# Optimization experiments

Hardware: AMD Instinct MI355X
Metric: run time of the kernel (lower is better)

The kernel has to match this reference:

```python
import jax, jax.numpy as jnp
import numpy as np

D_MODEL = 1024
NUM_HEADS = 16
D_K = D_MODEL // NUM_HEADS
SCALE = 1.0 / np.sqrt(D_K).astype(np.float32)
MASK_FILL = -10000.0


def setup_inputs() -> dict:
    key = jax.random.key(0)
    ks = jax.random.split(key, 5)
    B, S = 2, 2048
    x = jax.random.normal(ks[0], (B, S, D_MODEL), dtype=jnp.float32)
    mask = jax.random.randint(ks[1], (B, S), 0, 2, dtype=jnp.int32)
    # Kaiming-uniform-ish init like nn.Linear defaults
    lim1 = 1.0 / np.sqrt(D_MODEL)
    Wqkv = jax.random.uniform(ks[2], (D_MODEL, 3 * D_MODEL), jnp.float32, -lim1, lim1)
    bqkv = jnp.zeros((3 * D_MODEL,), jnp.float32)
    Wout = jax.random.uniform(ks[3], (D_MODEL, D_MODEL), jnp.float32, -lim1, lim1)
    bout = jnp.zeros((D_MODEL,), jnp.float32)
    return {"x": x, "mask": mask, "Wqkv": Wqkv, "bqkv": bqkv, "Wout": Wout, "bout": bout}


def reference(x, mask, Wqkv, bqkv, Wout, bout):
    B, S, _ = x.shape
    qkv = (x @ Wqkv + bqkv).reshape(B, S, 3, NUM_HEADS, D_K)
    qkv = jnp.transpose(qkv, (2, 0, 3, 1, 4))
    q, k, v = qkv[0], qkv[1], qkv[2]
    # scaled dot-product scores [B,H,S,S]
    scores = jnp.einsum("bhqd,bhkd->bhqk", q, k) * SCALE
    # key-padding mask [B,S] -> [B,1,1,S]; masked positions set to -10000 (as in source)
    m = mask[:, None, None, :]
    scores = jnp.where(m == 0, MASK_FILL, scores)
    attn = jax.nn.softmax(scores, axis=-1)
    # dropout is disabled (eval/inference)
    context = jnp.einsum("bhqk,bhkd->bhqd", attn, v)
    context = jnp.transpose(context, (0, 2, 1, 3)).reshape(B, S, D_MODEL)
    return context @ Wout + bout
```

## Files before the change

### kernel.cpp

```cpp
#include <hip/hip_runtime.h>

typedef _Float16 f16;
typedef _Float16 f16x2 __attribute__((ext_vector_type(2)));
typedef _Float16 f16x4 __attribute__((ext_vector_type(4)));
typedef _Float16 f16x8 __attribute__((ext_vector_type(8)));
typedef float    f32x4 __attribute__((ext_vector_type(4)));
typedef float    f32x16 __attribute__((ext_vector_type(16)));
typedef int      i32x4 __attribute__((ext_vector_type(4)));

#define NHEADS 16
#define DK 64
#define BATCH 2
#define SEQ 2048
#define DMODEL 1024
#define MTOT (BATCH*SEQ)
#define NQKV (3*DMODEL)
#define NBH  (BATCH*NHEADS)
#define LOG2E 1.44269504f
#define QSCALE (0.125f * LOG2E)
#define MASKVAL (-10000.0f * LOG2E)

__device__ inline f16x8 ld_f16x8_g(const f16* p) {
  return __builtin_bit_cast(f16x8, *reinterpret_cast<const i32x4*>(p));
}

__device__ inline f16x2 cvt_pk(float a, float b) {
  return __builtin_bit_cast(f16x2, __builtin_amdgcn_cvt_pkrtz(a, b));
}

__device__ inline void gl_lds16(const void* g, void* l) {
  __builtin_amdgcn_global_load_lds(
      (const __attribute__((address_space(1))) unsigned int*)g,
      (__attribute__((address_space(3))) unsigned int*)l, 16, 0, 0);
}

__device__ inline int sigma_k(int s) {
  return (s & ~12) | ((s & 4) << 1) | ((s & 8) >> 1);
}

__device__ inline void tcvt_tile(float (*tile)[33], const float* __restrict__ in,
                                 f16* __restrict__ out, int K, int N, int k0, int n0) {
  const int t = threadIdx.x, tx = t & 31, ty = t >> 5;
  #pragma unroll
  for (int i = 0; i < 4; ++i)
    tile[ty + 8*i][tx] = in[(size_t)(k0 + ty + 8*i) * N + n0 + tx];
  __syncthreads();
  #pragma unroll
  for (int i = 0; i < 4; ++i)
    out[(size_t)(n0 + ty + 8*i) * K + k0 + tx] = (f16)tile[tx][ty + 8*i];
}

__global__ __launch_bounds__(256) void k_prep(
    const float* __restrict__ x, f16* __restrict__ xh,
    const float* __restrict__ Wqkv, f16* __restrict__ Wqkvt,
    const float* __restrict__ Wout, f16* __restrict__ Woutt,
    const int* __restrict__ mask, int* __restrict__ inv, int* __restrict__ cnt)
{
  __shared__ float tile[32][33];
  __shared__ int part[256];
  const int bid = blockIdx.x;
  const int t = threadIdx.x;
  if (bid < 4096) {
    int i = (bid * 256 + t) * 4;
    float4 v = *reinterpret_cast<const float4*>(x + i);
    f16x4 o = { (f16)v.x, (f16)v.y, (f16)v.z, (f16)v.w };
    *reinterpret_cast<f16x4*>(xh + i) = o;
  } else if (bid < 4096 + 3072) {
    int tl = bid - 4096;
    tcvt_tile(tile, Wqkv, Wqkvt, DMODEL, NQKV, (tl / 96) * 32, (tl % 96) * 32);
  } else if (bid < 8192) {
    int tl = bid - 4096 - 3072;
    tcvt_tile(tile, Wout, Woutt, DMODEL, DMODEL, (tl / 32) * 32, (tl % 32) * 32);
  } else {
    const int b = bid - 8192;
    const int* mp = mask + b * SEQ;
    int* iv = inv + b * SEQ;
    const int base = t * 8;
    int m[8]; int s = 0;
    #pragma unroll
    for (int i = 0; i < 8; ++i) { m[i] = mp[base + i]; s += (m[i] != 0); }
    part[t] = s;
    __syncthreads();
    for (int d = 1; d < 256; d <<= 1) {
      int v = (t >= d) ? part[t - d] : 0;
      __syncthreads();
      part[t] += v;
      __syncthreads();
    }
    int pos = (t == 0) ? 0 : part[t - 1];
    #pragma unroll
    for (int i = 0; i < 8; ++i) {
      if (m[i] != 0) { iv[pos] = base + i; ++pos; }
    }
    if (t == 255) cnt[b] = part[255];
  }
}

__global__ __launch_bounds__(256, 2) void k_gemm_qkv2(
    const f16* __restrict__ A, const f16* __restrict__ Bt,
    const float* __restrict__ bias, const int* __restrict__ inv,
    const int* __restrict__ cnt,
    f16* __restrict__ qo, f16* __restrict__ ko, f16* __restrict__ vto, int K)
{
  __shared__ f16 As[64][64];
  __shared__ f16 Bs[128][64];
  const int bid = blockIdx.x;
  const bool isQ = bid < 512;

  const int t = threadIdx.x;
  const int l = t & 63, w = t >> 6;
  const int lc = l & 15, g = l >> 4;
  const int srow = l >> 3;
  const int ssl  = ((l & 7) ^ srow) * 16;
  const int swz  = (lc & 7) << 4;

  int m0, n0, b = 0, c = 0;
  const f16* Btp;
  const float* biasp;
  size_t aoff[2];
  if (isQ) {
    n0 = (bid & 7) * 128;  m0 = (bid >> 3) * 64;
    Btp = Bt;  biasp = bias;
    #pragma unroll
    for (int it = 0; it < 2; ++it)
      aoff[it] = (size_t)(m0 + it*32 + w*8 + srow) * K;
  } else {
    const int idx = bid - 512;
    n0 = (idx & 15) * 128;  m0 = (idx >> 4) * 64;
    b = m0 >> 11;
    const int sl0 = m0 & (SEQ - 1);
    c = cnt[b];
    if (sl0 >= ((c + 63) & ~63)) return;
    Btp = Bt + (size_t)DMODEL * DMODEL;
    biasp = bias + DMODEL;
    #pragma unroll
    for (int it = 0; it < 2; ++it) {
      int slot = sl0 + it*32 + w*8 + srow;
      int sidx = (slot < c) ? slot : (c > 0 ? c - 1 : 0);
      aoff[it] = (size_t)(b * SEQ + (inv[b * SEQ + sidx] & (SEQ - 1))) * K;
    }
  }

  f32x4 acc[4][2] = {};

  for (int kt = 0; kt < K; kt += 64) {
    __syncthreads();
    #pragma unroll
    for (int it = 0; it < 2; ++it)
      gl_lds16((const char*)(A + aoff[it] + kt) + ssl, &As[it*32 + w*8][0]);
    #pragma unroll
    for (int it = 0; it < 4; ++it) {
      int row = it*32 + w*8 + srow;
      gl_lds16((const char*)(Btp + (size_t)(n0 + row) * K + kt) + ssl,
               &Bs[it*32 + w*8][0]);
    }
    __syncthreads();

    #pragma unroll
    for (int ks = 0; ks < 64; ks += 32) {
      f16x8 af[4], bf[2];
      #pragma unroll
      for (int i = 0; i < 4; ++i)
        af[i] = *(const f16x8*)((const char*)&As[i*16 + lc][0] + ((ks*2 + g*16) ^ swz));
      #pragma unroll
      for (int j = 0; j < 2; ++j)
        bf[j] = *(const f16x8*)((const char*)&Bs[w*32 + j*16 + lc][0] + ((ks*2 + g*16) ^ swz));
      #pragma unroll
      for (int i = 0; i < 4; ++i)
        #pragma unroll
        for (int j = 0; j < 2; ++j)
          acc[i][j] = __builtin_amdgcn_mfma_f32_16x16x32_f16(af[i], bf[j], acc[i][j], 0, 0, 0);
    }
  }

  if (isQ) {
    #pragma unroll
    for (int i = 0; i < 4; ++i) {
      const int row0 = m0 + i*16 + g*4;
      const int qb = row0 >> 11, s0 = row0 & (SEQ - 1);
      #pragma unroll
      for (int j = 0; j < 2; ++j) {
        int col = n0 + w*32 + j*16 + lc;
        float bv = biasp[col];
        int h = col >> 6, d = col & 63;
        size_t bh = (size_t)(qb * NHEADS + h);
        #pragma unroll
        for (int r = 0; r < 4; ++r)
          qo[(bh * SEQ + s0 + r) * DK + d] = (f16)((acc[i][j][r] + bv) * QSCALE);
      }
    }
  } else {
    const int sl0 = m0 & (SEQ - 1);
    #pragma unroll
    for (int i = 0; i < 4; ++i) {
      const int slot0 = sl0 + i*16 + g*4;
      #pragma unroll
      for (int j = 0; j < 2; ++j) {
        int colkv = n0 + w*32 + j*16 + lc;
        float bv = biasp[colkv];
        int kv = colkv >> 10;
        int h = (colkv >> 6) & 15, d = colkv & 63;
        size_t bh = (size_t)(b * NHEADS + h);
        if (kv == 0) {
          #pragma unroll
          for (int r = 0; r < 4; ++r)
            ko[(bh * SEQ + slot0 + r) * DK + d] = (f16)(acc[i][j][r] + bv);
        } else {
          union { f16x2 h2[2]; f16x4 h4; } u;
          u.h2[0] = cvt_pk(acc[i][j][0] + bv, acc[i][j][1] + bv);
          u.h2[1] = cvt_pk(acc[i][j][2] + bv, acc[i][j][3] + bv);
          *(f16x4*)(vto + (bh * DK + d) * SEQ + sigma_k(slot0)) = u.h4;
        }
      }
    }
  }
}

__global__ __launch_bounds__(256, 2) void k_gemm_out(
    const f16* __restrict__ A, const f16* __restrict__ Bt,
    const float* __restrict__ bias, float* __restrict__ outf, int N, int K)
{
  __shared__ f16 As[64][64];
  __shared__ f16 Bs[128][64];
  const int m0 = blockIdx.y * 64, n0 = blockIdx.x * 128;
  const int t = threadIdx.x;
  const int l = t & 63, w = t >> 6;
  const int lc = l & 15, g = l >> 4;
  const int srow = l >> 3;
  const int ssl  = ((l & 7) ^ srow) * 16;
  const int swz  = (lc & 7) << 4;

  f32x4 acc[4][2] = {};

  for (int kt = 0; kt < K; kt += 64) {
    __syncthreads();
    #pragma unroll
    for (int it = 0; it < 2; ++it) {
      int row = it*32 + w*8 + srow;
      gl_lds16((const char*)(A + (size_t)(m0 + row) * K + kt) + ssl,
               &As[it*32 + w*8][0]);
    }
    #pragma unroll
    for (int it = 0; it < 4; ++it) {
      int row = it*32 + w*8 + srow;
      gl_lds16((const char*)(Bt + (size_t)(n0 + row) * K + kt) + ssl,
               &Bs[it*32 + w*8][0]);
    }
    __syncthreads();

    #pragma unroll
    for (int ks = 0; ks < 64; ks += 32) {
      f16x8 af[4], bf[2];
      #pragma unroll
      for (int i = 0; i < 4; ++i)
        af[i] = *(const f16x8*)((const char*)&As[i*16 + lc][0] + ((ks*2 + g*16) ^ swz));
      #pragma unroll
      for (int j = 0; j < 2; ++j)
        bf[j] = *(const f16x8*)((const char*)&Bs[w*32 + j*16 + lc][0] + ((ks*2 + g*16) ^ swz));
      #pragma unroll
      for (int i = 0; i < 4; ++i)
        #pragma unroll
        for (int j = 0; j < 2; ++j)
          acc[i][j] = __builtin_amdgcn_mfma_f32_16x16x32_f16(af[i], bf[j], acc[i][j], 0, 0, 0);
    }
  }

  #pragma unroll
  for (int i = 0; i < 4; ++i) {
    #pragma unroll
    for (int j = 0; j < 2; ++j) {
      int col = n0 + w*32 + j*16 + lc;
      float bv = bias[col];
      #pragma unroll
      for (int r = 0; r < 4; ++r) {
        int row = m0 + i*16 + g*4 + r;
        outf[(size_t)row * N + col] = acc[i][j][r] + bv;
      }
    }
  }
}

__global__ __launch_bounds__(256, 2) void k_attn10(
    const f16* __restrict__ Q, const f16* __restrict__ K,
    const f16* __restrict__ Vt, const int* __restrict__ cnt,
    f16* __restrict__ ctx)
{
  __shared__ f16 Kb[2][32][128];
  __shared__ f16 Vb[2][32][128];

  const int bid = blockIdx.x;
  const int xcd = bid & 7, slot = bid >> 3;
  const int bh = xcd * 4 + (slot >> 4);
  const int qb = slot & 15;
  const int b  = bh >> 4, h = bh & (NHEADS - 1);
  const int t = threadIdx.x, l = t & 63, w = t >> 6;
  const int r31 = l & 31, hi = l >> 5;
  const int Rm = r31 & 15;
  const int q0 = qb * 128 + w * 32;

  const int c = cnt[b];
  const int NTc = (c + 63) >> 6;

  const f16* Qp = Q + (size_t)bh * SEQ * DK;
  const f16* Kp = K + (size_t)bh * SEQ * DK;
  const f16* Vp = Vt + (size_t)bh * DK * SEQ;

  f16x8 qf[4];
  #pragma unroll
  for (int ds = 0; ds < 4; ++ds)
    qf[ds] = ld_f16x8_g(Qp + (size_t)(q0 + r31) * DK + ds*16 + hi*8);

  f32x16 o[2] = {};
  float mrow = -3e38f;
  float lsum = 0.f;

  auto stage = [&](int buf, int kt) {
    #pragma unroll
    for (int cc = 0; cc < 2; ++cc) {
      int Rbase = w*8 + cc*4;
      int R = Rbase + (l >> 4);
      int u = (l & 15) ^ (R & 15);
      int off32 = (u >> 3) * 32;
      int byteoff = (u & 7) * 16;
      gl_lds16((const char*)Kp + (size_t)(kt + off32 + R) * (DK*2) + byteoff,
               &Kb[buf][Rbase][0]);
      gl_lds16((const char*)Vp + (size_t)(off32 + R) * (SEQ*2) + (size_t)kt*2 + byteoff,
               &Vb[buf][Rbase][0]);
    }
  };

  stage(0, 0);

  for (int it = 0; it < NTc; ++it) {
    __syncthreads();
    if (it + 1 < NTc) stage((it + 1) & 1, (it + 1) * 64);
    const int kt = it * 64;
    const char* kb = (const char*)&Kb[it & 1][0][0];
    const char* vb = (const char*)&Vb[it & 1][0][0];

    f32x16 p[2];
    if (kt + 64 <= c) {
      #pragma unroll
      for (int T = 0; T < 2; ++T)
        #pragma unroll
        for (int r = 0; r < 16; ++r) p[T][r] = 0.f;
    } else {
      #pragma unroll
      for (int T = 0; T < 2; ++T)
        #pragma unroll
        for (int r = 0; r < 16; ++r) {
          int k = kt + T*32 + 4*hi + (r & 3) + 8*(r >> 2);
          p[T][r] = (k < c) ? 0.f : MASKVAL;
        }
    }

    __builtin_amdgcn_s_setprio(1);
    #pragma unroll
    for (int T = 0; T < 2; ++T)
      #pragma unroll
      for (int ds = 0; ds < 4; ++ds) {
        int slotc = T*8 + ds*2 + hi;
        f16x8 kf = *(const f16x8*)(kb + r31*256 + ((slotc ^ Rm) << 4));
        p[T] = __builtin_amdgcn_mfma_f32_32x32x16_f16(kf, qf[ds], p[T], 0, 0, 0);
      }
    __builtin_amdgcn_s_setprio(0);

    float mx;
    {
      f32x4 t4;
      #pragma unroll
      for (int r = 0; r < 4; ++r)
        t4[r] = fmaxf(fmaxf(p[0][r], p[0][r+4]), fmaxf(p[0][r+8], p[0][r+12]));
      #pragma unroll
      for (int r = 0; r < 4; ++r)
        t4[r] = fmaxf(t4[r], fmaxf(fmaxf(p[1][r], p[1][r+4]), fmaxf(p[1][r+8], p[1][r+12])));
      mx = fmaxf(fmaxf(t4[0], t4[1]), fmaxf(t4[2], t4[3]));
    }
    mx = fmaxf(mx, __shfl_xor(mx, 32));

    if (!__all(mx <= mrow + 8.f)) {
      float nm = fmaxf(mrow, mx);
      float sc = __builtin_amdgcn_exp2f(mrow - nm);
      mrow = nm;
      lsum *= sc;
      #pragma unroll
      for (int dt = 0; dt < 2; ++dt)
        #pragma unroll
        for (int r = 0; r < 16; ++r) o[dt][r] *= sc;
    }

    f16x2 h2[2][8];
    float s0 = 0.f, s1 = 0.f;
    #pragma unroll
    for (int T = 0; T < 2; ++T)
      #pragma unroll
      for (int rp = 0; rp < 8; ++rp) {
        float e0 = __builtin_amdgcn_exp2f(p[T][2*rp]   - mrow);
        float e1 = __builtin_amdgcn_exp2f(p[T][2*rp+1] - mrow);
        s0 += e0; s1 += e1;
        h2[T][rp] = cvt_pk(e0, e1);
      }
    lsum += s0 + s1;

    __builtin_amdgcn_s_setprio(1);
    #pragma unroll
    for (int T = 0; T < 2; ++T)
      #pragma unroll
      for (int half = 0; half < 2; ++half) {
        union { f16x2 a[4]; f16x8 v8; } pu;
        pu.a[0] = h2[T][half*4+0]; pu.a[1] = h2[T][half*4+1];
        pu.a[2] = h2[T][half*4+2]; pu.a[3] = h2[T][half*4+3];
        int m = T*2 + half;
        #pragma unroll
        for (int dt = 0; dt < 2; ++dt) {
          int slotc = dt*8 + m*2 + hi;
          f16x8 vf = *(const f16x8*)(vb + r31*256 + ((slotc ^ Rm) << 4));
          o[dt] = __builtin_amdgcn_mfma_f32_32x32x16_f16(vf, pu.v8, o[dt], 0, 0, 0);
        }
      }
    __builtin_amdgcn_s_setprio(0);
  }

  lsum += __shfl_xor(lsum, 32);
  float inv = 1.f / lsum;
  f16* cp = ctx + (size_t)(b*SEQ + q0 + r31) * DMODEL + h*DK;
  #pragma unroll
  for (int dt = 0; dt < 2; ++dt)
    #pragma unroll
    for (int rq = 0; rq < 4; ++rq) {
      union { f16x2 h2v[2]; f16x4 h4v; } u;
      u.h2v[0] = cvt_pk(o[dt][4*rq+0]*inv, o[dt][4*rq+1]*inv);
      u.h2v[1] = cvt_pk(o[dt][4*rq+2]*inv, o[dt][4*rq+3]*inv);
      *(f16x4*)(cp + dt*32 + 8*rq + 4*hi) = u.h4v;
    }
}

extern "C" void kernel_launch(void* const* d_in, const int* in_sizes, int n_in,
                              void* d_out, int out_size, void* d_ws, size_t ws_size,
                              hipStream_t stream) {
  const float* x    = (const float*)d_in[0];
  const int*   mask = (const int*)d_in[1];
  const float* Wqkv = (const float*)d_in[2];
  const float* bqkv = (const float*)d_in[3];
  const float* Wout = (const float*)d_in[4];
  const float* bout = (const float*)d_in[5];
  float* out = (float*)d_out;

  const size_t SZ_X    = (size_t)MTOT * DMODEL * 2;
  const size_t SZ_WQKV = (size_t)NQKV * DMODEL * 2;
  const size_t SZ_WOUT = (size_t)DMODEL * DMODEL * 2;
  const size_t SZ_QKV  = (size_t)BATCH * NHEADS * SEQ * DK * 2;
  const size_t SZ_INV  = (size_t)MTOT * 4;
  const size_t SZ_CNT  = 256;
  const size_t NEED = SZ_X + SZ_WQKV + SZ_WOUT + 3*SZ_QKV + SZ_X + SZ_INV + SZ_CNT;
  if (ws_size < NEED) return;

  char* p = (char*)d_ws;
  f16* xh    = (f16*)p; p += SZ_X;
  f16* Wqkvt = (f16*)p; p += SZ_WQKV;
  f16* Woutt = (f16*)p; p += SZ_WOUT;
  f16* Qh    = (f16*)p; p += SZ_QKV;
  f16* Kh    = (f16*)p; p += SZ_QKV;
  f16* Vth   = (f16*)p; p += SZ_QKV;
  f16* ctx   = (f16*)p; p += SZ_X;
  int* inv   = (int*)p; p += SZ_INV;
  int* cnt   = (int*)p; p += SZ_CNT;

  k_prep<<<4096 + 3072 + 1024 + BATCH, 256, 0, stream>>>(
      x, xh, Wqkv, Wqkvt, Wout, Woutt, mask, inv, cnt);

  k_gemm_qkv2<<<512 + 1024, 256, 0, stream>>>(
      xh, Wqkvt, bqkv, inv, cnt, Qh, Kh, Vth, DMODEL);

  k_attn10<<<32 * 16, 256, 0, stream>>>(Qh, Kh, Vth, cnt, ctx);

  k_gemm_out<<<dim3(DMODEL/128, MTOT/64), 256, 0, stream>>>(
      ctx, Woutt, bout, out, DMODEL, DMODEL);
}
```

Measured before the change: 97.73 us.

## Double-buffer GEMM LDS tiles, widen attention staging, vectorize weight transpose

Both GEMM kernels get double-buffered LDS with a prefetch of the next K tile issued before computing the current one, which cuts one barrier per iteration and overlaps global loads with MFMA work. The attention kernel now stages two 64-key tiles per period, halving barrier count, and the weight transpose-convert uses float4 loads and packed f16x4 stores. In exchange, LDS per block doubles in every kernel (48KB for the GEMMs, 64KB for attention), which may limit occupancy.

```diff
diff --git a/kernel.cpp b/kernel.cpp
--- a/kernel.cpp
+++ b/kernel.cpp
@@ -40,14 +40,15 @@
 
 __device__ inline void tcvt_tile(float (*tile)[33], const float* __restrict__ in,
                                  f16* __restrict__ out, int K, int N, int k0, int n0) {
-  const int t = threadIdx.x, tx = t & 31, ty = t >> 5;
-  #pragma unroll
-  for (int i = 0; i < 4; ++i)
-    tile[ty + 8*i][tx] = in[(size_t)(k0 + ty + 8*i) * N + n0 + tx];
+  const int t = threadIdx.x, j = t & 7, ty = t >> 3;
+  float4 v = *reinterpret_cast<const float4*>(in + (size_t)(k0 + ty) * N + n0 + j*4);
+  tile[ty][j*4+0] = v.x; tile[ty][j*4+1] = v.y;
+  tile[ty][j*4+2] = v.z; tile[ty][j*4+3] = v.w;
   __syncthreads();
-  #pragma unroll
-  for (int i = 0; i < 4; ++i)
-    out[(size_t)(n0 + ty + 8*i) * K + k0 + tx] = (f16)tile[tx][ty + 8*i];
+  union { f16x2 h2[2]; f16x4 h4; } u;
+  u.h2[0] = cvt_pk(tile[j*4+0][ty], tile[j*4+1][ty]);
+  u.h2[1] = cvt_pk(tile[j*4+2][ty], tile[j*4+3][ty]);
+  *(f16x4*)(out + (size_t)(n0 + ty) * K + k0 + j*4) = u.h4;
 }
 
 __global__ __launch_bounds__(256) void k_prep(
@@ -102,8 +103,8 @@
     const int* __restrict__ cnt,
     f16* __restrict__ qo, f16* __restrict__ ko, f16* __restrict__ vto, int K)
 {
-  __shared__ f16 As[64][64];
-  __shared__ f16 Bs[128][64];
+  __shared__ f16 As[2][64][64];
+  __shared__ f16 Bs[2][128][64];
   const int bid = blockIdx.x;
   const bool isQ = bid < 512;
 
@@ -141,30 +142,36 @@
     }
   }
 
-  f32x4 acc[4][2] = {};
-
-  for (int kt = 0; kt < K; kt += 64) {
-    __syncthreads();
+  auto stage = [&](int buf, int kt) {
     #pragma unroll
     for (int it = 0; it < 2; ++it)
-      gl_lds16((const char*)(A + aoff[it] + kt) + ssl, &As[it*32 + w*8][0]);
+      gl_lds16((const char*)(A + aoff[it] + kt) + ssl, &As[buf][it*32 + w*8][0]);
     #pragma unroll
     for (int it = 0; it < 4; ++it) {
       int row = it*32 + w*8 + srow;
       gl_lds16((const char*)(Btp + (size_t)(n0 + row) * K + kt) + ssl,
-               &Bs[it*32 + w*8][0]);
-    }
+               &Bs[buf][it*32 + w*8][0]);
+    }
+  };
+
+  f32x4 acc[4][2] = {};
+  const int NTk = K >> 6;
+  stage(0, 0);
+
+  for (int ti = 0; ti < NTk; ++ti) {
     __syncthreads();
-
+    if (ti + 1 < NTk) stage((ti + 1) & 1, (ti + 1) * 64);
+    const char* abase = (const char*)&As[ti & 1][0][0];
+    const char* bbase = (const char*)&Bs[ti & 1][0][0];
     #pragma unroll
     for (int ks = 0; ks < 64; ks += 32) {
       f16x8 af[4], bf[2];
       #pragma unroll
       for (int i = 0; i < 4; ++i)
-        af[i] = *(const f16x8*)((const char*)&As[i*16 + lc][0] + ((ks*2 + g*16) ^ swz));
+        af[i] = *(const f16x8*)(abase + (i*16 + lc)*128 + ((ks*2 + g*16) ^ swz));
       #pragma unroll
       for (int j = 0; j < 2; ++j)
-        bf[j] = *(const f16x8*)((const char*)&Bs[w*32 + j*16 + lc][0] + ((ks*2 + g*16) ^ swz));
+        bf[j] = *(const f16x8*)(bbase + (w*32 + j*16 + lc)*128 + ((ks*2 + g*16) ^ swz));
       #pragma unroll
       for (int i = 0; i < 4; ++i)
         #pragma unroll
@@ -220,8 +227,8 @@
     const f16* __restrict__ A, const f16* __restrict__ Bt,
     const float* __restrict__ bias, float* __restrict__ outf, int N, int K)
 {
-  __shared__ f16 As[64][64];
-  __shared__ f16 Bs[128][64];
+  __shared__ f16 As[2][64][64];
+  __shared__ f16 Bs[2][128][64];
   const int m0 = blockIdx.y * 64, n0 = blockIdx.x * 128;
   const int t = threadIdx.x;
   const int l = t & 63, w = t >> 6;
@@ -230,33 +237,39 @@
   const int ssl  = ((l & 7) ^ srow) * 16;
   const int swz  = (lc & 7) << 4;
 
-  f32x4 acc[4][2] = {};
-
-  for (int kt = 0; kt < K; kt += 64) {
-    __syncthreads();
+  auto stage = [&](int buf, int kt) {
     #pragma unroll
     for (int it = 0; it < 2; ++it) {
       int row = it*32 + w*8 + srow;
       gl_lds16((const char*)(A + (size_t)(m0 + row) * K + kt) + ssl,
-               &As[it*32 + w*8][0]);
+               &As[buf][it*32 + w*8][0]);
     }
     #pragma unroll
     for (int it = 0; it < 4; ++it) {
       int row = it*32 + w*8 + srow;
       gl_lds16((const char*)(Bt + (size_t)(n0 + row) * K + kt) + ssl,
-               &Bs[it*32 + w*8][0]);
-    }
+               &Bs[buf][it*32 + w*8][0]);
+    }
+  };
+
+  f32x4 acc[4][2] = {};
+  const int NTk = K >> 6;
+  stage(0, 0);
+
+  for (int ti = 0; ti < NTk; ++ti) {
     __syncthreads();
-
+    if (ti + 1 < NTk) stage((ti + 1) & 1, (ti + 1) * 64);
+    const char* abase = (const char*)&As[ti & 1][0][0];
+    const char* bbase = (const char*)&Bs[ti & 1][0][0];
     #pragma unroll
     for (int ks = 0; ks < 64; ks += 32) {
       f16x8 af[4], bf[2];
       #pragma unroll
       for (int i = 0; i < 4; ++i)
-        af[i] = *(const f16x8*)((const char*)&As[i*16 + lc][0] + ((ks*2 + g*16) ^ swz));
+        af[i] = *(const f16x8*)(abase + (i*16 + lc)*128 + ((ks*2 + g*16) ^ swz));
       #pragma unroll
       for (int j = 0; j < 2; ++j)
-        bf[j] = *(const f16x8*)((const char*)&Bs[w*32 + j*16 + lc][0] + ((ks*2 + g*16) ^ swz));
+        bf[j] = *(const f16x8*)(bbase + (w*32 + j*16 + lc)*128 + ((ks*2 + g*16) ^ swz));
       #pragma unroll
       for (int i = 0; i < 4; ++i)
         #pragma unroll
@@ -280,13 +293,13 @@
   }
 }
 
-__global__ __launch_bounds__(256, 2) void k_attn10(
+__global__ __launch_bounds__(256, 2) void k_attn11(
     const f16* __restrict__ Q, const f16* __restrict__ K,
     const f16* __restrict__ Vt, const int* __restrict__ cnt,
     f16* __restrict__ ctx)
 {
-  __shared__ f16 Kb[2][32][128];
-  __shared__ f16 Vb[2][32][128];
+  __shared__ f16 Kb[2][2][32][128];
+  __shared__ f16 Vb[2][2][32][128];
 
   const int bid = blockIdx.x;
   const int xcd = bid & 7, slot = bid >> 3;
@@ -300,6 +313,7 @@
 
   const int c = cnt[b];
   const int NTc = (c + 63) >> 6;
+  const int NP  = (NTc + 1) >> 1;
 
   const f16* Qp = Q + (size_t)bh * SEQ * DK;
   const f16* Kp = K + (size_t)bh * SEQ * DK;
@@ -314,111 +328,124 @@
   float mrow = -3e38f;
   float lsum = 0.f;
 
-  auto stage = [&](int buf, int kt) {
-    #pragma unroll
-    for (int cc = 0; cc < 2; ++cc) {
-      int Rbase = w*8 + cc*4;
-      int R = Rbase + (l >> 4);
-      int u = (l & 15) ^ (R & 15);
-      int off32 = (u >> 3) * 32;
-      int byteoff = (u & 7) * 16;
-      gl_lds16((const char*)Kp + (size_t)(kt + off32 + R) * (DK*2) + byteoff,
-               &Kb[buf][Rbase][0]);
-      gl_lds16((const char*)Vp + (size_t)(off32 + R) * (SEQ*2) + (size_t)kt*2 + byteoff,
-               &Vb[buf][Rbase][0]);
+  auto stage_period = [&](int buf, int pp) {
+    #pragma unroll
+    for (int j2 = 0; j2 < 2; ++j2) {
+      int tile = pp*2 + j2;
+      if (tile >= NTc) break;
+      int kt = tile * 64;
+      #pragma unroll
+      for (int cc = 0; cc < 2; ++cc) {
+        int Rbase = w*8 + cc*4;
+        int R = Rbase + (l >> 4);
+        int u = (l & 15) ^ (R & 15);
+        int off32 = (u >> 3) * 32;
+        int byteoff = (u & 7) * 16;
+        gl_lds16((const char*)Kp + (size_t)(kt + off32 + R) * (DK*2) + byteoff,
+                 &Kb[buf][j2][Rbase][0]);
+        gl_lds16((const char*)Vp + (size_t)(off32 + R) * (SEQ*2) + (size_t)kt*2 + byteoff,
+                 &Vb[buf][j2][Rbase][0]);
+      }
     }
   };
 
-  stage(0, 0);
-
-  for (int it = 0; it < NTc; ++it) {
+  stage_period(0, 0);
+
+  for (int pp = 0; pp < NP; ++pp) {
     __syncthreads();
-    if (it + 1 < NTc) stage((it + 1) & 1, (it + 1) * 64);
-    const int kt = it * 64;
-    const char* kb = (const char*)&Kb[it & 1][0][0];
-    const char* vb = (const char*)&Vb[it & 1][0][0];
-
-    f32x16 p[2];
-    if (kt + 64 <= c) {
+    if (pp + 1 < NP) stage_period((pp + 1) & 1, pp + 1);
+    const int buf = pp & 1;
+
+    #pragma unroll
+    for (int j2 = 0; j2 < 2; ++j2) {
+      const int tile = pp*2 + j2;
+      if (tile >= NTc) break;
+      const int kt = tile * 64;
+      const char* kb = (const char*)&Kb[buf][j2][0][0];
+      const char* vb = (const char*)&Vb[buf][j2][0][0];
+
+      f32x16 p[2];
+      if (kt + 64 <= c) {
+        #pragma unroll
+        for (int T = 0; T < 2; ++T)
+          #pragma unroll
+          for (int r = 0; r < 16; ++r) p[T][r] = 0.f;
+      } else {
+        #pragma unroll
+        for (int T = 0; T < 2; ++T)
+          #pragma unroll
+          for (int r = 0; r < 16; ++r) {
+            int k = kt + T*32 + 4*hi + (r & 3) + 8*(r >> 2);
+            p[T][r] = (k < c) ? 0.f : MASKVAL;
+          }
+      }
+
+      __builtin_amdgcn_s_setprio(1);
       #pragma unroll
       for (int T = 0; T < 2; ++T)
         #pragma unroll
-        for (int r = 0; r < 16; ++r) p[T][r] = 0.f;
-    } else {
+        for (int ds = 0; ds < 4; ++ds) {
+          int slotc = T*8 + ds*2 + hi;
+          f16x8 kf = *(const f16x8*)(kb + r31*256 + ((slotc ^ Rm) << 4));
+          p[T] = __builtin_amdgcn_mfma_f32_32x32x16_f16(kf, qf[ds], p[T], 0, 0, 0);
+        }
+      __builtin_amdgcn_s_setprio(0);
+
+      float mx;
+      {
+        f32x4 t4;
+        #pragma unroll
+        for (int r = 0; r < 4; ++r)
+          t4[r] = fmaxf(fmaxf(p[0][r], p[0][r+4]), fmaxf(p[0][r+8], p[0][r+12]));
+        #pragma unroll
+        for (int r = 0; r < 4; ++r)
+          t4[r] = fmaxf(t4[r], fmaxf(fmaxf(p[1][r], p[1][r+4]), fmaxf(p[1][r+8], p[1][r+12])));
+        mx = fmaxf(fmaxf(t4[0], t4[1]), fmaxf(t4[2], t4[3]));
+      }
+      mx = fmaxf(mx, __shfl_xor(mx, 32));
+
+      if (!__all(mx <= mrow + 8.f)) {
+        float nm = fmaxf(mrow, mx);
+        float sc = __builtin_amdgcn_exp2f(mrow - nm);
+        mrow = nm;
+        lsum *= sc;
+        #pragma unroll
+        for (int dt = 0; dt < 2; ++dt)
+          #pragma unroll
+          for (int r = 0; r < 16; ++r) o[dt][r] *= sc;
+      }
+
+      f16x2 h2[2][8];
+      float s0 = 0.f, s1 = 0.f;
       #pragma unroll
       for (int T = 0; T < 2; ++T)
         #pragma unroll
-        for (int r = 0; r < 16; ++r) {
-          int k = kt + T*32 + 4*hi + (r & 3) + 8*(r >> 2);
-          p[T][r] = (k < c) ? 0.f : MASKVAL;
+        for (int rp = 0; rp < 8; ++rp) {
+          float e0 = __builtin_amdgcn_exp2f(p[T][2*rp]   - mrow);
+          float e1 = __builtin_amdgcn_exp2f(p[T][2*rp+1] - mrow);
+          s0 += e0; s1 += e1;
+          h2[T][rp] = cvt_pk(e0, e1);
         }
-    }
-
-    __builtin_amdgcn_s_setprio(1);
-    #pragma unroll
-    for (int T = 0; T < 2; ++T)
-      #pragma unroll
-      for (int ds = 0; ds < 4; ++ds) {
-        int slotc = T*8 + ds*2 + hi;
-        f16x8 kf = *(const f16x8*)(kb + r31*256 + ((slotc ^ Rm) << 4));
-        p[T] = __builtin_amdgcn_mfma_f32_32x32x16_f16(kf, qf[ds], p[T], 0, 0, 0);
-      }
-    __builtin_amdgcn_s_setprio(0);
-
-    float mx;
-    {
-      f32x4 t4;
-      #pragma unroll
-      for (int r = 0; r < 4; ++r)
-        t4[r] = fmaxf(fmaxf(p[0][r], p[0][r+4]), fmaxf(p[0][r+8], p[0][r+12]));
-      #pragma unroll
-      for (int r = 0; r < 4; ++r)
-        t4[r] = fmaxf(t4[r], fmaxf(fmaxf(p[1][r], p[1][r+4]), fmaxf(p[1][r+8], p[1][r+12])));
-      mx = fmaxf(fmaxf(t4[0], t4[1]), fmaxf(t4[2], t4[3]));
-    }
-    mx = fmaxf(mx, __shfl_xor(mx, 32));
-
-    if (!__all(mx <= mrow + 8.f)) {
-      float nm = fmaxf(mrow, mx);
-      float sc = __builtin_amdgcn_exp2f(mrow - nm);
-      mrow = nm;
-      lsum *= sc;
-      #pragma unroll
-      for (int dt = 0; dt < 2; ++dt)
-        #pragma unroll
-        for (int r = 0; r < 16; ++r) o[dt][r] *= sc;
-    }
-
-    f16x2 h2[2][8];
-    float s0 = 0.f, s1 = 0.f;
-    #pragma unroll
-    for (int T = 0; T < 2; ++T)
-      #pragma unroll
-      for (int rp = 0; rp < 8; ++rp) {
-        float e0 = __builtin_amdgcn_exp2f(p[T][2*rp]   - mrow);
-        float e1 = __builtin_amdgcn_exp2f(p[T][2*rp+1] - mrow);
-        s0 += e0; s1 += e1;
-        h2[T][rp] = cvt_pk(e0, e1);
-      }
-    lsum += s0 + s1;
-
-    __builtin_amdgcn_s_setprio(1);
-    #pragma unroll
-    for (int T = 0; T < 2; ++T)
-      #pragma unroll
-      for (int half = 0; half < 2; ++half) {
-        union { f16x2 a[4]; f16x8 v8; } pu;
-        pu.a[0] = h2[T][half*4+0]; pu.a[1] = h2[T][half*4+1];
-        pu.a[2] = h2[T][half*4+2]; pu.a[3] = h2[T][half*4+3];
-        int m = T*2 + half;
-        #pragma unroll
-        for (int dt = 0; dt < 2; ++dt) {
-          int slotc = dt*8 + m*2 + hi;
-          f16x8 vf = *(const f16x8*)(vb + r31*256 + ((slotc ^ Rm) << 4));
-          o[dt] = __builtin_amdgcn_mfma_f32_32x32x16_f16(vf, pu.v8, o[dt], 0, 0, 0);
+      lsum += s0 + s1;
+
+      __builtin_amdgcn_s_setprio(1);
+      #pragma unroll
+      for (int T = 0; T < 2; ++T)
+        #pragma unroll
+        for (int half = 0; half < 2; ++half) {
+          union { f16x2 a[4]; f16x8 v8; } pu;
+          pu.a[0] = h2[T][half*4+0]; pu.a[1] = h2[T][half*4+1];
+          pu.a[2] = h2[T][half*4+2]; pu.a[3] = h2[T][half*4+3];
+          int m = T*2 + half;
+          #pragma unroll
+          for (int dt = 0; dt < 2; ++dt) {
+            int slotc = dt*8 + m*2 + hi;
+            f16x8 vf = *(const f16x8*)(vb + r31*256 + ((slotc ^ Rm) << 4));
+            o[dt] = __builtin_amdgcn_mfma_f32_32x32x16_f16(vf, pu.v8, o[dt], 0, 0, 0);
+          }
         }
-      }
-    __builtin_amdgcn_s_setprio(0);
+      __builtin_amdgcn_s_setprio(0);
+    }
   }
 
   lsum += __shfl_xor(lsum, 32);
@@ -472,7 +499,7 @@
   k_gemm_qkv2<<<512 + 1024, 256, 0, stream>>>(
       xh, Wqkvt, bqkv, inv, cnt, Qh, Kh, Vth, DMODEL);
 
-  k_attn10<<<32 * 16, 256, 0, stream>>>(Qh, Kh, Vth, cnt, ctx);
+  k_attn11<<<32 * 16, 256, 0, stream>>>(Qh, Kh, Vth, cnt, ctx);
 
   k_gemm_out<<<dim3(DMODEL/128, MTOT/64), 256, 0, stream>>>(
       ctx, Woutt, bout, out, DMODEL, DMODEL);
```

After: 96.23 us. About the same (-1.5%).
